# Kernel tuning notes

Hardware: AMD Instinct MI355X
Metric: run time of the kernel (lower is better)

Reference implementation:

```python
import jax, jax.numpy as jnp
import numpy as np

N, D, S = 262144, 512, 8192
EPS = 0.006  # constant offset added in the original module


def setup_inputs() -> dict:
    key = jax.random.key(0)
    k1, k2 = jax.random.split(key)
    x = jax.random.normal(k1, (N, D), dtype=jnp.float32)
    # Build S contiguous, non-overlapping inclusive [start, end] boundaries
    cuts = jnp.sort(jax.random.randint(k2, (S - 1,), 1, N, dtype=jnp.int32))
    starts = jnp.concatenate([jnp.zeros((1,), jnp.int32), cuts])
    ends = jnp.concatenate([cuts, jnp.full((1,), N, jnp.int32)]) - 1
    ends = jnp.maximum(ends, starts)  # guard against empty segments
    graph = jnp.stack([starts, ends], axis=1)  # [S, 2] int32
    return {"input": x, "graph": graph}


def reference(input, graph):
    # Per-segment mean over rows start..end (inclusive), + 0.006.
    # Single-pass vectorized form via an exclusive prefix sum:
    #   sum(input[s:e+1]) = P[e+1] - P[s]
    P = jnp.concatenate(
        [jnp.zeros((1, input.shape[1]), input.dtype), jnp.cumsum(input, axis=0)],
        axis=0,
    )  # [N+1, D]
    starts = graph[:, 0]
    ends = graph[:, 1]
    seg_sum = P[ends + 1] - P[starts]  # [S, D]
    counts = (ends - starts + 1).astype(input.dtype)
    return seg_sum / counts[:, None] + jnp.asarray(EPS, input.dtype)
```

## Files before the change

### kernel.cpp

```cpp
#include <hip/hip_runtime.h>


#define EPS_VAL 0.006f
#define DIM 512
#define DV 128
#define TILE 128
#define GROUP 8
#define NGROUPS (TILE / GROUP)
#define MAXSEG 64

typedef float f32x4 __attribute__((ext_vector_type(4)));

__global__ __launch_bounds__(256) void init_kernel(
    f32x4* __restrict__ out, int n4,
    const int* __restrict__ graph, int* __restrict__ lo_arr,
    int ntiles, int S) {
  const int i = blockIdx.x * 256 + threadIdx.x;
  if (i < n4) out[i] = (f32x4){0.f, 0.f, 0.f, 0.f};
  if (i < ntiles) {
    const int r0 = i * TILE;
    int lo = 0, hi = S - 1;
    while (lo < hi) {
      int mid = (lo + hi) >> 1;
      if (graph[2 * mid + 1] < r0) lo = mid + 1; else hi = mid;
    }
    lo_arr[i] = lo;
  }
}

__global__ __launch_bounds__(128, 4) void pool_tile_kernel(
    const float* __restrict__ x,
    const int* __restrict__ graph,
    const int* __restrict__ lo_arr,
    float* __restrict__ out,
    int N, int S) {
  __shared__ int2 sdesc[MAXSEG];
  const int r0 = blockIdx.x * TILE;
  const int r1 = r0 + TILE - 1;
  const int t = threadIdx.x;

  const int lo = lo_arr[blockIdx.x];
  if (t < MAXSEG) {
    const int si = lo + t;
    sdesc[t] = (si < S) ? reinterpret_cast<const int2*>(graph)[si]
                        : make_int2(N, N);
  }
  __syncthreads();

  int s = lo;
  int seg_st = sdesc[0].x;
  int seg_en = sdesc[0].y;

  const f32x4* xp = reinterpret_cast<const f32x4*>(x) + (size_t)r0 * DV + t;

  f32x4 acc = (f32x4){0.f, 0.f, 0.f, 0.f};
  f32x4 buf[GROUP];
#pragma unroll
  for (int j = 0; j < GROUP; ++j) buf[j] = __builtin_nontemporal_load(xp + j * DV);
  xp += GROUP * DV;

#pragma unroll
  for (int g = 0; g < NGROUPS; ++g) {
    f32x4 nbuf[GROUP];
    if (g + 1 < NGROUPS) {
#pragma unroll
      for (int j = 0; j < GROUP; ++j) nbuf[j] = __builtin_nontemporal_load(xp + j * DV);
      xp += GROUP * DV;
    }
#pragma unroll
    for (int j = 0; j < GROUP; ++j) {
      const int r = r0 + g * GROUP + j;
      const f32x4 v = buf[j];
      acc += v;
      while (r == seg_en) {
        const float inv = 1.0f / (float)(seg_en - seg_st + 1);
        f32x4 res = acc * inv;
        float* op = out + (size_t)s * DIM + t * 4;
        if (seg_st >= r0) {
          res += EPS_VAL;
          *reinterpret_cast<f32x4*>(op) = res;
        } else {
          unsafeAtomicAdd(op + 0, res.x);
          unsafeAtomicAdd(op + 1, res.y);
          unsafeAtomicAdd(op + 2, res.z);
          unsafeAtomicAdd(op + 3, res.w);
        }
        ++s;
        const int widx = s - lo;
        int2 nx;
        if (widx < MAXSEG) {
          nx = sdesc[widx];
        } else {
          nx = (s < S) ? reinterpret_cast<const int2*>(graph)[s]
                       : make_int2(N, N);
        }
        seg_st = nx.x; seg_en = nx.y;
        if (seg_st <= r) { acc = v; }
        else { acc = (f32x4){0.f, 0.f, 0.f, 0.f}; }
      }
    }
#pragma unroll
    for (int j = 0; j < GROUP; ++j) buf[j] = nbuf[j];
  }

  if (s < S && seg_st <= r1) {
    const float inv = 1.0f / (float)(seg_en - seg_st + 1);
    f32x4 res = acc * inv;
    if (seg_st >= r0) {
      res += EPS_VAL;
    }
    float* op = out + (size_t)s * DIM + t * 4;
    unsafeAtomicAdd(op + 0, res.x);
    unsafeAtomicAdd(op + 1, res.y);
    unsafeAtomicAdd(op + 2, res.z);
    unsafeAtomicAdd(op + 3, res.w);
  }
}

extern "C" void kernel_launch(void* const* d_in, const int* in_sizes, int n_in,
                              void* d_out, int out_size, void* d_ws, size_t ws_size,
                              hipStream_t stream) {
  const float* x = (const float*)d_in[0];
  const int* graph = (const int*)d_in[1];
  float* out = (float*)d_out;
  int* lo_arr = (int*)d_ws;

  const int N = in_sizes[0] / DIM;
  const int S = in_sizes[1] / 2;
  const int ntiles = N / TILE;
  const int n4 = out_size / 4;

  const int init_items = (n4 > ntiles) ? n4 : ntiles;
  init_kernel<<<(init_items + 255) / 256, 256, 0, stream>>>(
      reinterpret_cast<f32x4*>(out), n4, graph, lo_arr, ntiles, S);

  pool_tile_kernel<<<ntiles, 128, 0, stream>>>(x, graph, lo_arr, out, N, S);
}
```

Before: 107.9 us.

## Assign segments to owning tile by start row, drop init kernel and atomics

Each block now owns the segments whose start row falls in its 128-row tile and reads past the tile boundary to finish them, so every output row is written once with a plain nontemporal store. This removes the zero-fill/binary-search init kernel and the cross-tile atomic adds. In exchange, load per block becomes uneven when segments are long, and each block does its own binary search over the graph at kernel start.

```diff
diff --git a/kernel.cpp b/kernel.cpp
--- a/kernel.cpp
+++ b/kernel.cpp
@@ -6,32 +6,13 @@
 #define DV 128
 #define TILE 128
 #define GROUP 8
-#define NGROUPS (TILE / GROUP)
 #define MAXSEG 64
 
 typedef float f32x4 __attribute__((ext_vector_type(4)));
 
-__global__ __launch_bounds__(256) void init_kernel(
-    f32x4* __restrict__ out, int n4,
-    const int* __restrict__ graph, int* __restrict__ lo_arr,
-    int ntiles, int S) {
-  const int i = blockIdx.x * 256 + threadIdx.x;
-  if (i < n4) out[i] = (f32x4){0.f, 0.f, 0.f, 0.f};
-  if (i < ntiles) {
-    const int r0 = i * TILE;
-    int lo = 0, hi = S - 1;
-    while (lo < hi) {
-      int mid = (lo + hi) >> 1;
-      if (graph[2 * mid + 1] < r0) lo = mid + 1; else hi = mid;
-    }
-    lo_arr[i] = lo;
-  }
-}
-
-__global__ __launch_bounds__(128, 4) void pool_tile_kernel(
+__global__ __launch_bounds__(128, 4) void pool_own_kernel(
     const float* __restrict__ x,
     const int* __restrict__ graph,
-    const int* __restrict__ lo_arr,
     float* __restrict__ out,
     int N, int S) {
   __shared__ int2 sdesc[MAXSEG];
@@ -39,82 +20,86 @@
   const int r1 = r0 + TILE - 1;
   const int t = threadIdx.x;
 
-  const int lo = lo_arr[blockIdx.x];
+  int lo = 0, hi = S;
+  while (lo < hi) {
+    int mid = (lo + hi) >> 1;
+    if (graph[2 * mid] < r0) lo = mid + 1; else hi = mid;
+  }
+
   if (t < MAXSEG) {
     const int si = lo + t;
     sdesc[t] = (si < S) ? reinterpret_cast<const int2*>(graph)[si]
-                        : make_int2(N, N);
+                        : make_int2(N + TILE, N + TILE);
   }
   __syncthreads();
 
-  int s = lo;
+  int nown = 0;
+  while (nown < MAXSEG && sdesc[nown].x <= r1) ++nown;
+  if (nown == 0) return;
+
+  const int rs = sdesc[0].x;
+  const int re = sdesc[nown - 1].y;
+  const int nm1 = N - 1;
+
+  const f32x4* x4 = reinterpret_cast<const f32x4*>(x);
+
+  int s = 0;
   int seg_st = sdesc[0].x;
   int seg_en = sdesc[0].y;
 
-  const f32x4* xp = reinterpret_cast<const f32x4*>(x) + (size_t)r0 * DV + t;
-
   f32x4 acc = (f32x4){0.f, 0.f, 0.f, 0.f};
   f32x4 buf[GROUP];
+
+#define LDROW(row) \
+  __builtin_nontemporal_load(x4 + (size_t)((row) < nm1 ? (row) : nm1) * DV + t)
+
+#define COMMIT(rr, v)                                                         \
+  while ((rr) == seg_en) {                                                    \
+    const float inv = 1.0f / (float)(seg_en - seg_st + 1);                    \
+    f32x4 res = acc * inv + EPS_VAL;                                          \
+    __builtin_nontemporal_store(                                              \
+        res, reinterpret_cast<f32x4*>(out + (size_t)(lo + s) * DIM) + t);     \
+    ++s;                                                                      \
+    int2 nx;                                                                  \
+    if (s < MAXSEG) nx = sdesc[s];                          \
+    else nx = (lo + s < S) ? reinterpret_cast<const int2*>(graph)[lo + s]     \
+                           : make_int2(N + TILE, N + TILE);                   \
+    seg_st = nx.x; seg_en = nx.y;                                             \
+    if (seg_st <= (rr)) acc = (v);                                            \
+    else acc = (f32x4){0.f, 0.f, 0.f, 0.f};                                   \
+  }
+
+  int r = rs;
 #pragma unroll
-  for (int j = 0; j < GROUP; ++j) buf[j] = __builtin_nontemporal_load(xp + j * DV);
-  xp += GROUP * DV;
+  for (int j = 0; j < GROUP; ++j) buf[j] = LDROW(r + j);
 
+  while (r + GROUP <= re + 1) {
+    f32x4 nbuf[GROUP];
 #pragma unroll
-  for (int g = 0; g < NGROUPS; ++g) {
-    f32x4 nbuf[GROUP];
-    if (g + 1 < NGROUPS) {
-#pragma unroll
-      for (int j = 0; j < GROUP; ++j) nbuf[j] = __builtin_nontemporal_load(xp + j * DV);
-      xp += GROUP * DV;
-    }
+    for (int j = 0; j < GROUP; ++j) nbuf[j] = LDROW(r + GROUP + j);
 #pragma unroll
     for (int j = 0; j < GROUP; ++j) {
-      const int r = r0 + g * GROUP + j;
+      const int rr = r + j;
       const f32x4 v = buf[j];
       acc += v;
-      while (r == seg_en) {
-        const float inv = 1.0f / (float)(seg_en - seg_st + 1);
-        f32x4 res = acc * inv;
-        float* op = out + (size_t)s * DIM + t * 4;
-        if (seg_st >= r0) {
-          res += EPS_VAL;
-          *reinterpret_cast<f32x4*>(op) = res;
-        } else {
-          unsafeAtomicAdd(op + 0, res.x);
-          unsafeAtomicAdd(op + 1, res.y);
-          unsafeAtomicAdd(op + 2, res.z);
-          unsafeAtomicAdd(op + 3, res.w);
-        }
-        ++s;
-        const int widx = s - lo;
-        int2 nx;
-        if (widx < MAXSEG) {
-          nx = sdesc[widx];
-        } else {
-          nx = (s < S) ? reinterpret_cast<const int2*>(graph)[s]
-                       : make_int2(N, N);
-        }
-        seg_st = nx.x; seg_en = nx.y;
-        if (seg_st <= r) { acc = v; }
-        else { acc = (f32x4){0.f, 0.f, 0.f, 0.f}; }
-      }
+      COMMIT(rr, v)
     }
 #pragma unroll
     for (int j = 0; j < GROUP; ++j) buf[j] = nbuf[j];
+    r += GROUP;
   }
 
-  if (s < S && seg_st <= r1) {
-    const float inv = 1.0f / (float)(seg_en - seg_st + 1);
-    f32x4 res = acc * inv;
-    if (seg_st >= r0) {
-      res += EPS_VAL;
+#pragma unroll
+  for (int j = 0; j < GROUP; ++j) {
+    const int rr = r + j;
+    if (rr <= re) {
+      const f32x4 v = buf[j];
+      acc += v;
+      COMMIT(rr, v)
     }
-    float* op = out + (size_t)s * DIM + t * 4;
-    unsafeAtomicAdd(op + 0, res.x);
-    unsafeAtomicAdd(op + 1, res.y);
-    unsafeAtomicAdd(op + 2, res.z);
-    unsafeAtomicAdd(op + 3, res.w);
   }
+#undef LDROW
+#undef COMMIT
 }
 
 extern "C" void kernel_launch(void* const* d_in, const int* in_sizes, int n_in,
@@ -123,16 +108,10 @@
   const float* x = (const float*)d_in[0];
   const int* graph = (const int*)d_in[1];
   float* out = (float*)d_out;
-  int* lo_arr = (int*)d_ws;
 
   const int N = in_sizes[0] / DIM;
   const int S = in_sizes[1] / 2;
   const int ntiles = N / TILE;
-  const int n4 = out_size / 4;
 
-  const int init_items = (n4 > ntiles) ? n4 : ntiles;
-  init_kernel<<<(init_items + 255) / 256, 256, 0, stream>>>(
-      reinterpret_cast<f32x4*>(out), n4, graph, lo_arr, ntiles, S);
-
-  pool_tile_kernel<<<ntiles, 128, 0, stream>>>(x, graph, lo_arr, out, N, S);
+  pool_own_kernel<<<ntiles, 128, 0, stream>>>(x, graph, out, N, S);
 }
```

New measurement: 120.8 us. 12.0% more time.
